# Performance work log

Hardware: AMD Instinct MI355X
Metric: run time of the kernel (lower is better)

Reference implementation:

```python
import jax, jax.numpy as jnp
import numpy as np

MIN_RATIO, MAX_RATIO = 0.7, 1.3
MIN_BIAS, MAX_BIAS = -4.0, 4.0
SOFTMAX_SCALE = 3.0


def setup_inputs() -> dict:
    key = jax.random.key(0)
    k1, k2, k3 = jax.random.split(key, 3)
    B, L_org, N = 32, 2048, 21
    org_tensor = jax.random.normal(k1, (B, L_org, N), dtype=jnp.float32)
    # small perturbations so the clamps are active but not saturated
    ratio_minus_one = 0.1 * jax.random.normal(k2, (N,), dtype=jnp.float32)
    bias = 0.5 * jax.random.normal(k3, (N,), dtype=jnp.float32)
    return {"org_tensor": org_tensor, "ratio_minus_one": ratio_minus_one,
            "bias": bias, "to_length": 2048}


def reference(org_tensor, ratio_minus_one, bias, to_length):
    # input_transformation with is_mark=False
    B, L_org, N = org_tensor.shape
    L_to = to_length
    dt = org_tensor.dtype
    # relu-based clamping in the original == clip
    ratio = jnp.clip(ratio_minus_one + 1.0, MIN_RATIO, MAX_RATIO)  # [N]
    b = jnp.clip(bias, MIN_BIAS, MAX_BIAS)                         # [N]
    org_pos = jnp.arange(-L_org, 0, dtype=dt)                      # [L_org]
    # transformed positions are batch-independent: [L_org, N, 1]
    tpos = org_pos[:, None, None] * ratio[None, :, None] + b[None, :, None]
    tgt = jnp.arange(-L_to, 0, dtype=dt)                           # [L_to]
    deltas = (tpos - tgt[None, None, :]) ** 2                      # [L_org, N, L_to]
    weights = jax.nn.softmax(-deltas * SOFTMAX_SCALE, axis=0)      # softmax over L_org
    # einsum 'bont,bon->btn' with batch-independent weights
    out = jnp.einsum('ont,bon->btn', weights, org_tensor)          # [B, L_to, N]
    return out
```

## Files before the change

kernel.cpp:

```cpp
#include <hip/hip_runtime.h>
#include <hip/hip_bf16.h>


constexpr int LORG  = 2048;
constexpr int LTO   = 2048;
constexpr int NCH   = 21;
constexpr int BATCH = 32;
constexpr int W     = 8;
constexpr int NW    = 2 * W + 1;
constexpr int TT    = 64;
constexpr int NBLK  = BATCH * (LTO / TT);

constexpr float MIN_RATIO = 0.7f, MAX_RATIO = 1.3f;
constexpr float MIN_BIAS  = -4.0f, MAX_BIAS = 4.0f;
constexpr float NEG3LOG2E = -3.0f * 1.4426950408889634f;

__device__ __forceinline__ int compute_o0(float tg, float bb, float ir) {
    const float ocf = (float)LORG + (tg - bb) * ir;
    int o0 = (int)floorf(ocf + 0.5f) - W;
    return max(0, min(LORG - NW, o0));
}

__global__ __launch_bounds__(256) void li_fused(
    const float* __restrict__ x,
    const float* __restrict__ rmo,
    const float* __restrict__ bias,
    float* __restrict__ out)
{
    const int h  = blockIdx.x;
    const int wk = (h & 7) * (NBLK / 8) + (h >> 3);
    const int b  = wk >> 5;
    const int tt = wk & 31;
    const int t0 = tt * TT;

    const int tid = threadIdx.x;
    const int tl  = tid & 63;
    const int wv  = tid >> 6;

    __shared__ float xs[NCH][128];
    __shared__ float osh[TT * NCH];
    __shared__ float rsh[NCH], bsh[NCH], irsh[NCH];
    __shared__ int   lov[NCH], lenv[NCH], order[NCH];

    if (tid < NCH) {
        const float r  = fminf(fmaxf(rmo[tid] + 1.0f, MIN_RATIO), MAX_RATIO);
        const float bb = fminf(fmaxf(bias[tid], MIN_BIAS), MAX_BIAS);
        const float ir = 1.0f / r;
        const int lo = compute_o0((float)(t0 - LTO), bb, ir);
        const int hi = compute_o0((float)(t0 + TT - 1 - LTO), bb, ir);
        rsh[tid]  = r;  bsh[tid] = bb;  irsh[tid] = ir;
        lov[tid]  = lo;
        lenv[tid] = hi + NW - lo;
    }
    __syncthreads();
    if (tid < NCH) {
        const int lo = lov[tid];
        int rank = 0;
        for (int mth = 0; mth < NCH; ++mth) {
            const int lm = lov[mth];
            rank += (lm < lo) || (lm == lo && mth < tid);
        }
        order[rank] = tid;
    }
    __syncthreads();

    for (int s = wv; s < NCH; s += 4) {
        const int n   = order[s];
        const int lo  = lov[n];
        const int len = lenv[n];
        const float* col = x + ((size_t)(b * LORG + lo)) * NCH + n;
        const int i0 = min(tl,      len - 1);
        const int i1 = min(tl + 64, len - 1);
        xs[n][tl]      = col[(size_t)i0 * NCH];
        xs[n][tl + 64] = col[(size_t)i1 * NCH];
    }

    const float tg = (float)(t0 + tl - LTO);
    for (int s = wv; s < NCH; s += 4) {
        const int n  = order[s];
        const float r  = rsh[n];
        const float bb = bsh[n];
        const float ir = irsh[n];
        const int   o0 = compute_o0(tg, bb, ir);
        const int base = o0 - lov[n];
        float d = (float)(o0 - LORG) * r + bb - tg;
        float js = floorf(-d * ir + 0.5f);
        js = fminf(fmaxf(js, 0.0f), 16.0f);
        const float dstar = d + js * r;
        const float m = NEG3LOG2E * dstar * dstar;
        float sum = 0.0f, acc = 0.0f;
        #pragma unroll
        for (int j = 0; j < NW; ++j) {
            const float wgt = exp2f(NEG3LOG2E * d * d - m);
            sum += wgt;
            acc = fmaf(wgt, xs[n][base + j], acc);
            d += r;
        }
        osh[tl * NCH + n] = acc * (1.0f / sum);
    }
    __syncthreads();

    float* dst = out + ((size_t)b * LTO + t0) * NCH;
    for (int i = tid; i < TT * NCH; i += 256) dst[i] = osh[i];
}

extern "C" void kernel_launch(void* const* d_in, const int* in_sizes, int n_in,
                              void* d_out, int out_size, void* d_ws, size_t ws_size,
                              hipStream_t stream) {
    const float* x    = (const float*)d_in[0];
    const float* rmo  = (const float*)d_in[1];
    const float* bias = (const float*)d_in[2];
    float* out = (float*)d_out;

    li_fused<<<NBLK, 256, 0, stream>>>(x, rmo, bias, out);
}
```

Baseline: 17.65 us.

## Partition work by input-row chunks with coalesced float4 loads instead of output tiles

Each block now owns a contiguous chunk of 64 input rows (plus a 16-row halo) and loads it into shared memory with coalesced float4 reads, replacing per-channel strided gathers. Each channel then scans the range of output positions whose window start falls in this chunk and writes results directly to global memory. This removes the strided input reads and the sort/staging of output, but the output writes are now scattered (strided by channel) and uncoalesced. Lanes also diverge where the chunk test skips positions, and per-channel output ranges are uneven.

```diff
diff --git a/kernel.cpp b/kernel.cpp
--- a/kernel.cpp
+++ b/kernel.cpp
@@ -8,8 +8,10 @@
 constexpr int BATCH = 32;
 constexpr int W     = 8;
 constexpr int NW    = 2 * W + 1;
-constexpr int TT    = 64;
-constexpr int NBLK  = BATCH * (LTO / TT);
+constexpr int C     = 64;
+constexpr int KMAX  = LORG / C;
+constexpr int RW    = C + 16;
+constexpr int NBLK  = BATCH * KMAX;
 
 constexpr float MIN_RATIO = 0.7f, MAX_RATIO = 1.3f;
 constexpr float MIN_BIAS  = -4.0f, MAX_BIAS = 4.0f;
@@ -21,7 +23,7 @@
     return max(0, min(LORG - NW, o0));
 }
 
-__global__ __launch_bounds__(256) void li_fused(
+__global__ __launch_bounds__(256) void li_chunk(
     const float* __restrict__ x,
     const float* __restrict__ rmo,
     const float* __restrict__ bias,
@@ -30,78 +32,62 @@
     const int h  = blockIdx.x;
     const int wk = (h & 7) * (NBLK / 8) + (h >> 3);
     const int b  = wk >> 5;
-    const int tt = wk & 31;
-    const int t0 = tt * TT;
+    const int kc = wk & 31;
+    const int ob = kc * C;
+    const int rows = min(RW, LORG - ob);
 
     const int tid = threadIdx.x;
-    const int tl  = tid & 63;
-    const int wv  = tid >> 6;
 
-    __shared__ float xs[NCH][128];
-    __shared__ float osh[TT * NCH];
+    __shared__ float xs[RW * NCH];
     __shared__ float rsh[NCH], bsh[NCH], irsh[NCH];
-    __shared__ int   lov[NCH], lenv[NCH], order[NCH];
+    __shared__ int   tlov[NCH], thiv[NCH];
 
     if (tid < NCH) {
         const float r  = fminf(fmaxf(rmo[tid] + 1.0f, MIN_RATIO), MAX_RATIO);
         const float bb = fminf(fmaxf(bias[tid], MIN_BIAS), MAX_BIAS);
-        const float ir = 1.0f / r;
-        const int lo = compute_o0((float)(t0 - LTO), bb, ir);
-        const int hi = compute_o0((float)(t0 + TT - 1 - LTO), bb, ir);
-        rsh[tid]  = r;  bsh[tid] = bb;  irsh[tid] = ir;
-        lov[tid]  = lo;
-        lenv[tid] = hi + NW - lo;
+        rsh[tid] = r;  bsh[tid] = bb;  irsh[tid] = 1.0f / r;
+        const float tauL = (float)LTO + bb + r * ((float)(ob     + W - LORG) - 0.5f);
+        const float tauH = (float)LTO + bb + r * ((float)(ob + C + W - LORG) - 0.5f);
+        int Tlo = (kc == 0)        ? 0   : max(0,   (int)ceilf(tauL) - 2);
+        int Thi = (kc == KMAX - 1) ? LTO : min(LTO, (int)ceilf(tauH) + 2);
+        tlov[tid] = Tlo;
+        thiv[tid] = Thi;
     }
-    __syncthreads();
-    if (tid < NCH) {
-        const int lo = lov[tid];
-        int rank = 0;
-        for (int mth = 0; mth < NCH; ++mth) {
-            const int lm = lov[mth];
-            rank += (lm < lo) || (lm == lo && mth < tid);
-        }
-        order[rank] = tid;
-    }
+
+    const float4* src = (const float4*)(x + ((size_t)b * LORG + ob) * NCH);
+    float4* xs4 = (float4*)xs;
+    const int nf4 = rows * NCH / 4;
+    for (int i = tid; i < nf4; i += 256) xs4[i] = src[i];
     __syncthreads();
 
-    for (int s = wv; s < NCH; s += 4) {
-        const int n   = order[s];
-        const int lo  = lov[n];
-        const int len = lenv[n];
-        const float* col = x + ((size_t)(b * LORG + lo)) * NCH + n;
-        const int i0 = min(tl,      len - 1);
-        const int i1 = min(tl + 64, len - 1);
-        xs[n][tl]      = col[(size_t)i0 * NCH];
-        xs[n][tl + 64] = col[(size_t)i1 * NCH];
-    }
-
-    const float tg = (float)(t0 + tl - LTO);
-    for (int s = wv; s < NCH; s += 4) {
-        const int n  = order[s];
+    const int wv   = tid >> 6;
+    const int lane = tid & 63;
+    for (int n = wv; n < NCH; n += 4) {
         const float r  = rsh[n];
         const float bb = bsh[n];
         const float ir = irsh[n];
-        const int   o0 = compute_o0(tg, bb, ir);
-        const int base = o0 - lov[n];
-        float d = (float)(o0 - LORG) * r + bb - tg;
-        float js = floorf(-d * ir + 0.5f);
-        js = fminf(fmaxf(js, 0.0f), 16.0f);
-        const float dstar = d + js * r;
-        const float m = NEG3LOG2E * dstar * dstar;
-        float sum = 0.0f, acc = 0.0f;
-        #pragma unroll
-        for (int j = 0; j < NW; ++j) {
-            const float wgt = exp2f(NEG3LOG2E * d * d - m);
-            sum += wgt;
-            acc = fmaf(wgt, xs[n][base + j], acc);
-            d += r;
+        const int Tlo = tlov[n], Thi = thiv[n];
+        for (int t = Tlo + lane; t < Thi; t += 64) {
+            const float tg = (float)(t - LTO);
+            const int   o0 = compute_o0(tg, bb, ir);
+            if ((o0 >> 6) != kc) continue;
+            const int base = o0 - ob;
+            float d = (float)(o0 - LORG) * r + bb - tg;
+            float js = floorf(-d * ir + 0.5f);
+            js = fminf(fmaxf(js, 0.0f), 16.0f);
+            const float ds = d + js * r;
+            const float m  = NEG3LOG2E * ds * ds;
+            float sum = 0.0f, acc = 0.0f;
+            #pragma unroll
+            for (int j = 0; j < NW; ++j) {
+                const float wgt = exp2f(NEG3LOG2E * d * d - m);
+                sum += wgt;
+                acc = fmaf(wgt, xs[(base + j) * NCH + n], acc);
+                d += r;
+            }
+            out[((size_t)b * LTO + t) * NCH + n] = acc * (1.0f / sum);
         }
-        osh[tl * NCH + n] = acc * (1.0f / sum);
     }
-    __syncthreads();
-
-    float* dst = out + ((size_t)b * LTO + t0) * NCH;
-    for (int i = tid; i < TT * NCH; i += 256) dst[i] = osh[i];
 }
 
 extern "C" void kernel_launch(void* const* d_in, const int* in_sizes, int n_in,
@@ -112,5 +98,5 @@
     const float* bias = (const float*)d_in[2];
     float* out = (float*)d_out;
 
-    li_fused<<<NBLK, 256, 0, stream>>>(x, rmo, bias, out);
+    li_chunk<<<NBLK, 256, 0, stream>>>(x, rmo, bias, out);
 }
```

Result: slower. 40.62 us (+130.1%).
